# Performance work log

Hardware: AMD Instinct MI355X
Metric: run time of the kernel (lower is better)

The kernel has to match this reference:

```python
import jax, jax.numpy as jnp
import numpy as np

SCALE = 0.08838834764831845  # 1/sqrt(128)
B, S, H, D = 16, 1, 16, 128
BLOCK_SIZE = 16
MAX_CTX = 1024
PROMPT_LEN = 512
NUM_BLOCKS = 2048
NEG_INF = -1e30


def setup_inputs() -> dict:
    key = jax.random.key(0)
    ks = jax.random.split(key, 8)
    hidden = H * D
    query = jax.random.normal(ks[0], (B, S, hidden), dtype=jnp.float32)
    k_new = jax.random.normal(ks[1], (B, S, hidden), dtype=jnp.float32)
    v_new = jax.random.normal(ks[2], (B, S, hidden), dtype=jnp.float32)
    key_cache = jax.random.normal(ks[3], (NUM_BLOCKS, H, BLOCK_SIZE, D), dtype=jnp.float32)
    value_cache = jax.random.normal(ks[4], (NUM_BLOCKS, H, D, BLOCK_SIZE), dtype=jnp.float32)
    # disjoint physical blocks per sequence: 32 prompt blocks + 64 decode blocks
    n_tbl = PROMPT_LEN // BLOCK_SIZE + MAX_CTX // BLOCK_SIZE  # 96
    block_tables = jnp.arange(B * n_tbl, dtype=jnp.int32).reshape(B, n_tbl)
    context_lens = jax.random.randint(ks[5], (B,), 1, MAX_CTX + 1, dtype=jnp.int32)
    # slot for the newly generated token (position context_lens-1 in decode region)
    pt_len = PROMPT_LEN // BLOCK_SIZE
    pos = context_lens - 1
    blk = block_tables[jnp.arange(B), pt_len + pos // BLOCK_SIZE]
    slot_mapping = (blk * BLOCK_SIZE + pos % BLOCK_SIZE).astype(jnp.int32).reshape(B, 1)
    attn_bias = jax.random.normal(ks[6], (B, H, 1, MAX_CTX), dtype=jnp.float32) * 0.1
    return {"query": query, "key": k_new, "value": v_new,
            "key_cache": key_cache, "value_cache": value_cache,
            "slot_mapping": slot_mapping, "block_tables": block_tables,
            "context_lens": context_lens, "attn_bias": attn_bias,
            "max_prompt_len": PROMPT_LEN}


def reference(query, key, value, key_cache, value_cache, slot_mapping,
              block_tables, context_lens, attn_bias, max_prompt_len):
    b, s, hidden = query.shape
    q = query.reshape(b * s, H, D)
    k_new = key.reshape(b * s, H, D)
    v_new = value.reshape(b * s, H, D)
    bs = value_cache.shape[3]
    # reshape_and_cache: write new K/V into paged caches at slot_mapping[:, -1]
    slots = slot_mapping[:, -1]
    bi, off = slots // bs, slots % bs
    key_cache = key_cache.at[bi, :, off, :].set(k_new)
    value_cache = value_cache.at[bi, :, :, off].set(v_new)
    # drop prompt blocks from the block table
    pt_len = (int(max_prompt_len) + bs - 1) // bs
    bt = block_tables[:, pt_len:]                      # [B, nb]
    nb = bt.shape[1]
    K = nb * bs
    keys = key_cache[bt]                               # [B, nb, H, bs, D]
    keys = keys.transpose(0, 2, 1, 3, 4).reshape(b, H, K, D)
    vals = value_cache[bt]                             # [B, nb, H, D, bs]
    vals = vals.transpose(0, 2, 1, 4, 3).reshape(b, H, K, D)
    scores = jnp.einsum('bhd,bhkd->bhk', q.reshape(b, H, D), keys) * SCALE
    scores = scores + attn_bias.astype(jnp.float32)[:, :, 0, :K]
    valid = jnp.arange(K, dtype=jnp.int32)[None, :] < context_lens[:, None]
    scores = jnp.where(valid[:, None, :], scores, NEG_INF)
    probs = jax.nn.softmax(scores, axis=-1)
    out = jnp.einsum('bhk,bhkd->bhd', probs, vals)
    return out.reshape(b, s, hidden)
```

## Files before the change

### kernel.cpp

```cpp
#include <hip/hip_runtime.h>
#include <cstdint>

#define NH 16
#define HD 128
#define BS 16
#define NTBL 96
#define PT_OFF 32
#define NSPLIT 16
#define SPLIT_BLOCKS 4
#define QK_SCALE 0.08838834764831845f
#define NEG_INF -1e30f
#define NB 16

__global__ __launch_bounds__(256) void attn_split_kernel(
    const float* __restrict__ q,
    const float* __restrict__ key_cache,
    const float* __restrict__ value_cache,
    const int* __restrict__ block_tables,
    const int* __restrict__ context_lens,
    const float* __restrict__ attn_bias,
    float* __restrict__ ws)
{
    const int s = blockIdx.x, h = blockIdx.y, b = blockIdx.z;
    const int ctx = context_lens[b];
    const int cap = ctx - 1;
    const int nbc = (ctx + 14) >> 4;
    const int jb0 = s * SPLIT_BLOCKS;
    if (jb0 >= nbc) return;
    const int nbl = min(SPLIT_BLOCKS, nbc - jb0);

    __shared__ float sc[64];
    __shared__ float sp[64];
    __shared__ int   sbt[SPLIT_BLOCKS];
    __shared__ float outA[128], outB[128];

    const int tid = threadIdx.x;
    const int wave = tid >> 6, lane = tid & 63;
    const int half = lane >> 5, lq = lane & 31;

    if (tid < SPLIT_BLOCKS) sbt[tid] = block_tables[b*NTBL + PT_OFF + jb0 + tid];

    const float4 qv = *(const float4*)(q + (size_t)b*2048 + h*HD + lq*4);
    __syncthreads();

    if (wave < nbl) {
        const int blk = sbt[wave];
        const float4* kb = (const float4*)(key_cache + ((size_t)blk*NH + h)*2048);
        #pragma unroll
        for (int i = 0; i < 8; ++i) {
            const float4 kv = kb[i*64 + lane];
            float part = kv.x*qv.x + kv.y*qv.y + kv.z*qv.z + kv.w*qv.w;
            part += __shfl_xor(part, 1);
            part += __shfl_xor(part, 2);
            part += __shfl_xor(part, 4);
            part += __shfl_xor(part, 8);
            part += __shfl_xor(part, 16);
            if (lq == 0) sc[wave*16 + i*2 + half] = part;
        }
    }
    __syncthreads();

    const int pos = lane;
    const int gpos = jb0*16 + pos;
    const bool valid = gpos < cap;
    const float x = valid
        ? (sc[pos]*QK_SCALE + attn_bias[((size_t)b*NH + h)*1024 + gpos])
        : NEG_INF;
    float m = x;
    #pragma unroll
    for (int msk = 32; msk >= 1; msk >>= 1) m = fmaxf(m, __shfl_xor(m, msk));
    const float pexp = valid ? __expf(x - m) : 0.0f;
    float l = pexp;
    #pragma unroll
    for (int msk = 32; msk >= 1; msk >>= 1) l += __shfl_xor(l, msk);
    if (wave == 0) sp[lane] = pexp;
    __syncthreads();

    const int team = tid >> 7, d = tid & 127;
    float acc = 0.0f;
    for (int jl = team; jl < nbl; jl += 2) {
        const int blk = sbt[jl];
        const float4* vb = (const float4*)(value_cache + ((size_t)blk*NH + h)*2048 + d*16);
        const float4 v0 = vb[0], v1 = vb[1], v2 = vb[2], v3 = vb[3];
        const float* pr = sp + jl*16;
        acc += pr[0]*v0.x + pr[1]*v0.y + pr[2]*v0.z  + pr[3]*v0.w;
        acc += pr[4]*v1.x + pr[5]*v1.y + pr[6]*v1.z  + pr[7]*v1.w;
        acc += pr[8]*v2.x + pr[9]*v2.y + pr[10]*v2.z + pr[11]*v2.w;
        acc += pr[12]*v3.x + pr[13]*v3.y + pr[14]*v3.z + pr[15]*v3.w;
    }
    if (team == 0) outA[d] = acc; else outB[d] = acc;
    __syncthreads();

    float* wsp = ws + (((size_t)b*NH + h)*NSPLIT + s)*130;
    if (tid < 128) wsp[tid] = outA[tid] + outB[tid];
    if (tid == 0) { wsp[128] = m; wsp[129] = l; }
}

__global__ __launch_bounds__(128) void reduce_kernel(
    const float* __restrict__ ws,
    const float* __restrict__ q,
    const float* __restrict__ k_new,
    const float* __restrict__ v_new,
    const int* __restrict__ context_lens,
    const float* __restrict__ attn_bias,
    float* __restrict__ out)
{
    const int h = blockIdx.x, b = blockIdx.y, d = threadIdx.x;
    const int wave = d >> 6, lane = d & 63;
    const int ctx = context_lens[b];
    const int cap = ctx - 1;
    const int nbc = (ctx + 14) >> 4;
    const int nsv = (nbc + SPLIT_BLOCKS - 1) >> 2;

    const size_t qoff = (size_t)b*2048 + h*HD + d;
    const float qd = q[qoff], kd = k_new[qoff], vd = v_new[qoff];

    float p = qd * kd;
    #pragma unroll
    for (int msk = 32; msk >= 1; msk >>= 1) p += __shfl_xor(p, msk);
    __shared__ float s2[2];
    if (lane == 0) s2[wave] = p;
    __syncthreads();
    const float score_new = (s2[0] + s2[1]) * QK_SCALE
                          + attn_bias[((size_t)b*NH + h)*1024 + cap];

    const float* base = ws + ((size_t)b*NH + h)*NSPLIT*130;
    float M = score_new;
    for (int s = 0; s < nsv; ++s) M = fmaxf(M, base[s*130 + 128]);
    const float w = __expf(score_new - M);
    float L = w, acc = w * vd;
    for (int s = 0; s < nsv; ++s) {
        const float e = __expf(base[s*130 + 128] - M);
        L   += base[s*130 + 129] * e;
        acc += base[s*130 + d] * e;
    }
    out[qoff] = acc / L;
}

extern "C" void kernel_launch(void* const* d_in, const int* in_sizes, int n_in,
                              void* d_out, int out_size, void* d_ws, size_t ws_size,
                              hipStream_t stream) {
    (void)in_sizes; (void)n_in; (void)out_size; (void)ws_size;
    const float* q        = (const float*)d_in[0];
    const float* k_new    = (const float*)d_in[1];
    const float* v_new    = (const float*)d_in[2];
    const float* kcache   = (const float*)d_in[3];
    const float* vcache   = (const float*)d_in[4];
    const int* btables    = (const int*)d_in[6];
    const int* ctx_lens   = (const int*)d_in[7];
    const float* bias     = (const float*)d_in[8];
    float* ws  = (float*)d_ws;
    float* out = (float*)d_out;

    attn_split_kernel<<<dim3(NSPLIT, NH, NB), 256, 0, stream>>>(
        q, kcache, vcache, btables, ctx_lens, bias, ws);
    reduce_kernel<<<dim3(NH, NB), 128, 0, stream>>>(
        ws, q, k_new, v_new, ctx_lens, bias, out);
}
```

Before: 454.7 us.

## Prefetch V blocks and bias before QK so loads overlap score computation

The split kernel now issues the value-cache loads for both of a team's blocks, and the attention-bias load, at kernel start, before the key dot products and softmax. Block-table entries are read straight from global memory instead of being staged in shared memory, which removes one barrier. Launch bounds now request 4 blocks per CU. The aim is to hide V-load latency behind the QK and softmax phases, at the cost of holding 32 extra floats in registers per thread.

```diff
diff --git a/kernel.cpp b/kernel.cpp
--- a/kernel.cpp
+++ b/kernel.cpp
@@ -12,7 +12,7 @@
 #define NEG_INF -1e30f
 #define NB 16
 
-__global__ __launch_bounds__(256) void attn_split_kernel(
+__global__ __launch_bounds__(256, 4) void attn_split_kernel(
     const float* __restrict__ q,
     const float* __restrict__ key_cache,
     const float* __restrict__ value_cache,
@@ -31,21 +31,41 @@
 
     __shared__ float sc[64];
     __shared__ float sp[64];
-    __shared__ int   sbt[SPLIT_BLOCKS];
     __shared__ float outA[128], outB[128];
 
     const int tid = threadIdx.x;
     const int wave = tid >> 6, lane = tid & 63;
     const int half = lane >> 5, lq = lane & 31;
+    const int team = tid >> 7, d = tid & 127;
 
-    if (tid < SPLIT_BLOCKS) sbt[tid] = block_tables[b*NTBL + PT_OFF + jb0 + tid];
+    const int tbl = b*NTBL + PT_OFF + jb0;
 
     const float4 qv = *(const float4*)(q + (size_t)b*2048 + h*HD + lq*4);
-    __syncthreads();
 
-    if (wave < nbl) {
-        const int blk = sbt[wave];
-        const float4* kb = (const float4*)(key_cache + ((size_t)blk*NH + h)*2048);
+    const int gpos = jb0*16 + lane;
+    const bool valid = gpos < cap;
+    const float biasv = valid
+        ? attn_bias[((size_t)b*NH + h)*1024 + gpos] : 0.0f;
+
+    const bool vact0 = (team)     < nbl;
+    const bool vact1 = (team + 2) < nbl;
+    float4 v00 = {0,0,0,0}, v01 = {0,0,0,0}, v02 = {0,0,0,0}, v03 = {0,0,0,0};
+    float4 v10 = {0,0,0,0}, v11 = {0,0,0,0}, v12 = {0,0,0,0}, v13 = {0,0,0,0};
+    if (vact0) {
+        const int blk = block_tables[tbl + team];
+        const float4* vb = (const float4*)(value_cache + ((size_t)blk*NH + h)*2048 + d*16);
+        v00 = vb[0]; v01 = vb[1]; v02 = vb[2]; v03 = vb[3];
+    }
+    if (vact1) {
+        const int blk = block_tables[tbl + team + 2];
+        const float4* vb = (const float4*)(value_cache + ((size_t)blk*NH + h)*2048 + d*16);
+        v10 = vb[0]; v11 = vb[1]; v12 = vb[2]; v13 = vb[3];
+    }
+
+    const bool kact = wave < nbl;
+    if (kact) {
+        const int kblk = block_tables[tbl + wave];
+        const float4* kb = (const float4*)(key_cache + ((size_t)kblk*NH + h)*2048);
         #pragma unroll
         for (int i = 0; i < 8; ++i) {
             const float4 kv = kb[i*64 + lane];
@@ -60,12 +80,7 @@
     }
     __syncthreads();
 
-    const int pos = lane;
-    const int gpos = jb0*16 + pos;
-    const bool valid = gpos < cap;
-    const float x = valid
-        ? (sc[pos]*QK_SCALE + attn_bias[((size_t)b*NH + h)*1024 + gpos])
-        : NEG_INF;
+    const float x = valid ? (sc[lane]*QK_SCALE + biasv) : NEG_INF;
     float m = x;
     #pragma unroll
     for (int msk = 32; msk >= 1; msk >>= 1) m = fmaxf(m, __shfl_xor(m, msk));
@@ -76,17 +91,20 @@
     if (wave == 0) sp[lane] = pexp;
     __syncthreads();
 
-    const int team = tid >> 7, d = tid & 127;
     float acc = 0.0f;
-    for (int jl = team; jl < nbl; jl += 2) {
-        const int blk = sbt[jl];
-        const float4* vb = (const float4*)(value_cache + ((size_t)blk*NH + h)*2048 + d*16);
-        const float4 v0 = vb[0], v1 = vb[1], v2 = vb[2], v3 = vb[3];
-        const float* pr = sp + jl*16;
-        acc += pr[0]*v0.x + pr[1]*v0.y + pr[2]*v0.z  + pr[3]*v0.w;
-        acc += pr[4]*v1.x + pr[5]*v1.y + pr[6]*v1.z  + pr[7]*v1.w;
-        acc += pr[8]*v2.x + pr[9]*v2.y + pr[10]*v2.z + pr[11]*v2.w;
-        acc += pr[12]*v3.x + pr[13]*v3.y + pr[14]*v3.z + pr[15]*v3.w;
+    if (vact0) {
+        const float* pr = sp + team*16;
+        acc += pr[0]*v00.x  + pr[1]*v00.y  + pr[2]*v00.z  + pr[3]*v00.w;
+        acc += pr[4]*v01.x  + pr[5]*v01.y  + pr[6]*v01.z  + pr[7]*v01.w;
+        acc += pr[8]*v02.x  + pr[9]*v02.y  + pr[10]*v02.z + pr[11]*v02.w;
+        acc += pr[12]*v03.x + pr[13]*v03.y + pr[14]*v03.z + pr[15]*v03.w;
+    }
+    if (vact1) {
+        const float* pr = sp + (team+2)*16;
+        acc += pr[0]*v10.x  + pr[1]*v10.y  + pr[2]*v10.z  + pr[3]*v10.w;
+        acc += pr[4]*v11.x  + pr[5]*v11.y  + pr[6]*v11.z  + pr[7]*v11.w;
+        acc += pr[8]*v12.x  + pr[9]*v12.y  + pr[10]*v12.z + pr[11]*v12.w;
+        acc += pr[12]*v13.x + pr[13]*v13.y + pr[14]*v13.z + pr[15]*v13.w;
     }
     if (team == 0) outA[d] = acc; else outB[d] = acc;
     __syncthreads();
```

Result: no change. 453.6 us (-0.2%).
